# Optimization experiments

Measured on AMD Instinct MI355X. Metric: run time of the kernel, lower is better.

Reference implementation:

```python
import jax, jax.numpy as jnp
import numpy as np

BATCH, HIDDEN, DIM_X, N_FORCING, DIM_T, MODES = 16, 128, 128, 4, 64, 96


def setup_inputs() -> dict:
    key = jax.random.key(0)
    k1, k2, k3, k4, k5 = jax.random.split(key, 5)
    scale = 1.0 / HIDDEN ** 2
    return {
        "z0": jax.random.normal(k1, (BATCH, HIDDEN, DIM_X), jnp.float32),
        "xi": jax.random.normal(k2, (BATCH, N_FORCING, DIM_X, DIM_T), jnp.float32),
        "A": scale * jax.random.uniform(k3, (2, MODES, HIDDEN, HIDDEN), jnp.float32),
        "W_F": jax.random.normal(k4, (HIDDEN, HIDDEN), jnp.float32) / np.sqrt(HIDDEN).astype(np.float32),
        "W_G": jax.random.normal(k5, (HIDDEN, N_FORCING, HIDDEN), jnp.float32) / np.sqrt(HIDDEN).astype(np.float32),
    }


def _spde_func(z, W_F, W_G):
    # z: (b, h, x) -> F_z: (b, h, x), G_z: (b, h, n, x)
    F_z = jnp.tanh(jnp.einsum('oh,bhx->box', W_F, z))
    G_z = jnp.tanh(jnp.einsum('onh,bhx->bonx', W_G, z))
    return F_z, G_z


def _compl_mat_vec_mul_1d(A, z):
    # A: (2, modes, h, h); z: (batch, 2, modes, h) -- (real, imag) stacked on dim 1
    op = lambda M, u: jnp.einsum('xij,bxj->bxi', M, u)
    re = op(A[0], z[:, 0]) - op(A[1], z[:, 1])
    im = op(A[1], z[:, 0]) - op(A[0], z[:, 1])  # faithful to original (minus sign)
    return jnp.stack([re, im], axis=1)


def _prod(v, xi_t, A, W_F, W_G, a, b):
    # v: (batch, 2, dim_x, hidden); xi_t: (batch, dim_x, n_forcing) = dX/dt at step i
    Av = jnp.zeros_like(v).at[:, :, a:b].set(_compl_mat_vec_mul_1d(A, v[:, :, a:b]))
    vc = v[:, 0] + 1j * v[:, 1]                      # (b, x, h) complex
    z = jnp.fft.ifft(jnp.fft.ifftshift(vc, axes=1), axis=1).real  # (b, x, h)
    z = jnp.transpose(z, (0, 2, 1))                  # (b, h, x)
    F_z, G_z = _spde_func(z, W_F, W_G)
    G_z_xi = jnp.einsum('bhnx,bxn->bhx', G_z, xi_t)
    H = F_z + G_z_xi                                 # (b, h, x)
    hf = jnp.fft.fftshift(jnp.fft.fft(H, axis=2), axes=2)
    hf = jnp.stack([hf.real, hf.imag], axis=1)       # (b, 2, h, x)
    hf = jnp.transpose(hf, (0, 1, 3, 2))             # (b, 2, x, h)
    out_ft = jnp.zeros_like(v).at[:, :, a:b].set(hf[:, :, a:b])
    return Av + out_ft


def reference(z0, xi, A, W_F, W_G):
    batch, hidden, dim_x = z0.shape
    modes = A.shape[1]
    a, b = dim_x // 2 - modes // 2, dim_x // 2 + modes // 2
    # v0: band-limited shifted FFT of z0, layout (b, 2, x, h)
    z0_ft = jnp.fft.fftshift(jnp.fft.fft(z0, axis=2), axes=2)
    z0_ft = jnp.stack([z0_ft.real, z0_ft.imag], axis=1)            # (b, 2, h, x)
    v0 = jnp.zeros_like(z0_ft).at[:, :, :, a:b].set(z0_ft[:, :, :, a:b])
    v0 = jnp.transpose(v0, (0, 1, 3, 2))                           # (b, 2, x, h)
    # control increments: linear interp slope on uniform grid t=arange(T), dt=1
    xi_path = jnp.transpose(xi, (0, 2, 3, 1))                      # (b, x, t, n)
    dxi = xi_path[:, :, 1:, :] - xi_path[:, :, :-1, :]             # (b, x, t-1, n)
    dxi = jnp.moveaxis(dxi, 2, 0)                                  # (t-1, b, x, n)

    def step(v, d):
        v_new = v + _prod(v, d, A, W_F, W_G, a, b)  # Euler, dt = 1
        return v_new, v_new

    _, traj = jax.lax.scan(step, v0, dxi)                          # (t-1, b, 2, x, h)
    traj = jnp.concatenate([v0[None], traj], axis=0)               # (t, b, 2, x, h)
    vc = traj[:, :, 0] + 1j * traj[:, :, 1]                        # (t, b, x, h)
    vc = jnp.transpose(vc, (1, 3, 2, 0))                           # (b, h, x, t)
    z = jnp.fft.ifft(jnp.fft.ifftshift(vc, axes=2), axis=2).real   # (b, h, x, t)
    return z
```

## Files before the change

### kernel.cpp

```cpp
#include <hip/hip_runtime.h>
#include <math.h>

#define BATCH 16
#define HID   128
#define NX    128
#define NF    4
#define NT    64
#define MODES 96
#define NWG   256
#define TPB   1024
#define GSZ   16
#define ZSZ   ((size_t)BATCH * NX * HID)

__global__ void k_tables(float* __restrict__ C, float* __restrict__ S,
                         float2* __restrict__ T2m) {
    int m = blockIdx.x, x = threadIdx.x;
    if (x < NX) {
        int k = (80 + m) % NX;
        float ang = (float)((k * x) & (NX - 1)) * (2.0f * (float)M_PI / (float)NX);
        float c = cosf(ang), s = sinf(ang);
        C[m * NX + x] = c;
        S[m * NX + x] = s;
        T2m[m * NX + x] = make_float2(c, s);
    }
}

__global__ void k_dxi(const float* __restrict__ xi, float* __restrict__ dxi) {
    int idx = blockIdx.x * blockDim.x + threadIdx.x;
    const int total = (NT - 1) * BATCH * NX * NF;
    if (idx < total) {
        int n = idx & (NF - 1);
        int x = (idx >> 2) & (NX - 1);
        int b = (idx >> 9) & (BATCH - 1);
        int t = idx >> 13;
        const float* base = xi + (((size_t)b * NF + n) * NX + x) * NT;
        dxi[idx] = base[t + 1] - base[t];
    }
}

__global__ void k_wt4(const float* __restrict__ WF, const float* __restrict__ WGm,
                      float4* __restrict__ Wt4, float* __restrict__ Wt1) {
    int idx = blockIdx.x * 256 + threadIdx.x;
    if (idx < 16 * HID * 8) {
        int ol = idx & 7, h = (idx >> 3) & 127, j = idx >> 10;
        int o = j * 8 + ol;
        Wt4[idx] = make_float4(WF[(size_t)o * HID + h],
                               WGm[((size_t)o * NF + 0) * HID + h],
                               WGm[((size_t)o * NF + 1) * HID + h],
                               WGm[((size_t)o * NF + 2) * HID + h]);
        Wt1[idx] = WGm[((size_t)o * NF + 3) * HID + h];
    }
}

__global__ void k_at2(const float* __restrict__ A, float2* __restrict__ At2) {
    __shared__ float t0[32][33], t1[32][33];
    int m = blockIdx.z;
    int h0 = blockIdx.x * 32, o0 = blockIdx.y * 32;
    int tx = threadIdx.x, ty = threadIdx.y;
    const float* A0 = A + (size_t)m * HID * HID;
    const float* A1 = A0 + (size_t)MODES * HID * HID;
    #pragma unroll
    for (int j = 0; j < 32; j += 8) {
        t0[ty + j][tx] = A0[(size_t)(o0 + ty + j) * HID + h0 + tx];
        t1[ty + j][tx] = A1[(size_t)(o0 + ty + j) * HID + h0 + tx];
    }
    __syncthreads();
    #pragma unroll
    for (int j = 0; j < 32; j += 8)
        At2[((size_t)m * HID + h0 + ty + j) * HID + o0 + tx] =
            make_float2(t0[tx][ty + j], t1[tx][ty + j]);
}

__global__ __launch_bounds__(TPB, 1) void k_solve(
    const float* __restrict__ z0, const float* __restrict__ Ct,
    const float* __restrict__ St, const float2* __restrict__ T2m,
    const float4* __restrict__ Wt4g, const float* __restrict__ Wt1g,
    const float2* __restrict__ At2, const float* __restrict__ dxi,
    float2* __restrict__ va, float2* __restrict__ vb,
    float* __restrict__ zbuf, float* __restrict__ Hc,
    float* __restrict__ out, int* __restrict__ barc)
{
    __shared__ float2 CS[MODES][8];
    __shared__ float  zsl[NX][132];
    __shared__ float4 Wsl4[HID][8];
    __shared__ float  Wsl1[HID][9];
    __shared__ float  dxs[NX][5];
    __shared__ float2 vsl[6][HID];

    const int w = blockIdx.x;
    const int t = threadIdx.x;
    const int b = w >> 4;
    const int j = w & 15;
    const int xg0 = j * 8;
    const int o0 = j * 8;
    const int m0 = j * 6;

    int nbar = 0;
    int* ctr = barc + b * 64;
    auto gbar = [&]() {
        ++nbar;
        __syncthreads();
        if (t == 0) {
            __hip_atomic_fetch_add(ctr, 1, __ATOMIC_RELEASE,
                                   __HIP_MEMORY_SCOPE_AGENT);
            while (__hip_atomic_load(ctr, __ATOMIC_RELAXED,
                                     __HIP_MEMORY_SCOPE_AGENT) < GSZ * nbar)
                __builtin_amdgcn_s_sleep(2);
            (void)__hip_atomic_load(ctr, __ATOMIC_ACQUIRE,
                                    __HIP_MEMORY_SCOPE_AGENT);
        }
        __syncthreads();
    };

    if (t < MODES * 8) {
        int m = t >> 3, xp = t & 7;
        CS[m][xp] = T2m[m * NX + xg0 + xp];
    }
    {
        int h = t >> 3, ol = t & 7;
        Wsl4[h][ol] = Wt4g[((size_t)j * HID + h) * 8 + ol];
        Wsl1[h][ol] = Wt1g[((size_t)j * HID + h) * 8 + ol];
    }

    {
        int h = t & 127, q = t >> 7;
        int c = q & 1, mq = q >> 1;
        const float* zr = z0 + ((size_t)b * HID + h) * NX;
        float* fva = (float*)va;
        #pragma unroll
        for (int jj = 0; jj < 2; ++jj) {
            int mm = mq + 4 * jj;
            if (mm < 6) {
                int m = m0 + mm;
                const float* Trow = (c ? St : Ct) + m * NX;
                float acc = 0.f;
                #pragma unroll 4
                for (int x = 0; x < NX; ++x) acc += zr[x] * Trow[x];
                if (c) acc = -acc;
                fva[(((size_t)b * MODES + m) * HID + h) * 2 + c] = acc;
            }
        }
    }
    gbar();

    float2* vcur = va;
    float2* vnxt = vb;

    for (int step = 0; step < NT; ++step) {
        if (step > 0 && (step & 15) == 0) {
            int t0 = step - 16;
            int xl = t >> 7, h = t & 127;
            int x = xg0 + xl;
            float vals[16];
            #pragma unroll
            for (int tt = 0; tt < 16; ++tt)
                vals[tt] = zbuf[(size_t)tt * ZSZ + ((size_t)b * NX + x) * HID + h];
            float* dst = out + (((size_t)b * HID + h) * NX + x) * NT + t0;
            #pragma unroll
            for (int q = 0; q < 4; ++q)
                ((float4*)dst)[q] = make_float4(vals[q*4], vals[q*4+1],
                                                vals[q*4+2], vals[q*4+3]);
        }

        {
            int h = t & 127, xp = t >> 7;
            const float2* vr = vcur + (size_t)b * MODES * HID + h;
            float acc = 0.f;
            #pragma unroll 4
            for (int m = 0; m < MODES; ++m) {
                float2 vv = vr[(size_t)m * HID];
                float2 cs = CS[m][xp];
                acc += vv.x * cs.x - vv.y * cs.y;
            }
            acc *= 0.0078125f;
            zbuf[(size_t)(step & 15) * ZSZ + ((size_t)b * NX + xg0 + xp) * HID + h] = acc;
        }
        if (step == NT - 1) break;
        gbar();

        {
            const float4* z4 = (const float4*)(zbuf + (size_t)(step & 15) * ZSZ
                                               + (size_t)b * NX * HID);
            #pragma unroll
            for (int k = 0; k < 4; ++k) {
                int idx = t + k * 1024;
                int x = idx >> 5, h4 = (idx & 31) * 4;
                *(float4*)&zsl[x][h4] = z4[idx];
            }
            if (t < 512)
                dxs[t >> 2][t & 3] =
                    dxi[((size_t)step * BATCH + b) * NX * NF + t];
            __syncthreads();

            int ol = t & 7, x = t >> 3;
            float a0 = 0.f, a1 = 0.f, a2 = 0.f, a3 = 0.f, a4 = 0.f;
            #pragma unroll 4
            for (int h = 0; h < HID; ++h) {
                float zv = zsl[x][h];
                float4 w4 = Wsl4[h][ol];
                float w1 = Wsl1[h][ol];
                a0 += w4.x * zv; a1 += w4.y * zv;
                a2 += w4.z * zv; a3 += w4.w * zv;
                a4 += w1 * zv;
            }
            float hv = tanhf(a0)
                     + tanhf(a1) * dxs[x][0]
                     + tanhf(a2) * dxs[x][1]
                     + tanhf(a3) * dxs[x][2]
                     + tanhf(a4) * dxs[x][3];
            Hc[((size_t)b * NX + x) * HID + o0 + ol] = hv;
            __syncthreads();
        }
        gbar();

        {
            if (t < 6 * HID) {
                int ml = t >> 7, h = t & 127;
                vsl[ml][h] = vcur[((size_t)b * MODES + m0 + ml) * HID + h];
            }
            __syncthreads();
            if (t < 768) {
                int o = t & 127, ml = t >> 7;
                int m = m0 + ml;
                const float* hp = Hc + (size_t)b * NX * HID + o;
                const float2* trow = T2m + (size_t)m * NX;
                float fre = 0.f, fim = 0.f;
                #pragma unroll 4
                for (int x = 0; x < NX; ++x) {
                    float hv = hp[(size_t)x * HID];
                    float2 cs = trow[x];
                    fre += hv * cs.x;
                    fim -= hv * cs.y;
                }
                const float2* a2p = At2 + ((size_t)m * HID) * HID + o;
                float are = 0.f, aim = 0.f;
                #pragma unroll 4
                for (int h = 0; h < HID; ++h) {
                    float2 a = a2p[(size_t)h * HID];
                    float2 vv = vsl[ml][h];
                    are += a.x * vv.x - a.y * vv.y;
                    aim += a.y * vv.x - a.x * vv.y;
                }
                float2 vo = vsl[ml][o];
                vnxt[((size_t)b * MODES + m) * HID + o] =
                    make_float2(vo.x + are + fre, vo.y + aim + fim);
            }
            __syncthreads();
        }
        gbar();

        float2* tmp = vcur; vcur = vnxt; vnxt = tmp;
    }

    {
        int xl = t >> 7, h = t & 127;
        int x = xg0 + xl;
        float vals[16];
        #pragma unroll
        for (int tt = 0; tt < 16; ++tt)
            vals[tt] = zbuf[(size_t)tt * ZSZ + ((size_t)b * NX + x) * HID + h];
        float* dst = out + (((size_t)b * HID + h) * NX + x) * NT + 48;
        #pragma unroll
        for (int q = 0; q < 4; ++q)
            ((float4*)dst)[q] = make_float4(vals[q*4], vals[q*4+1],
                                            vals[q*4+2], vals[q*4+3]);
    }
}

extern "C" void kernel_launch(void* const* d_in, const int* in_sizes, int n_in,
                              void* d_out, int out_size, void* d_ws, size_t ws_size,
                              hipStream_t stream) {
    const float* z0 = (const float*)d_in[0];
    const float* xi = (const float*)d_in[1];
    const float* A  = (const float*)d_in[2];
    const float* WF = (const float*)d_in[3];
    const float* WG = (const float*)d_in[4];
    float* out = (float*)d_out;

    float* ws = (float*)d_ws;
    size_t off = 0;
    auto alloc = [&](size_t n) { float* p = ws + off; off += n; return p; };

    float*  Ct   = alloc((size_t)MODES * NX);
    float*  St   = alloc((size_t)MODES * NX);
    float2* T2m  = (float2*)alloc((size_t)MODES * NX * 2);
    float4* Wt4  = (float4*)alloc((size_t)16 * HID * 8 * 4);
    float*  Wt1  = alloc((size_t)16 * HID * 8);
    float2* At2  = (float2*)alloc((size_t)MODES * HID * HID * 2);
    float2* va   = (float2*)alloc((size_t)BATCH * MODES * HID * 2);
    float2* vb   = (float2*)alloc((size_t)BATCH * MODES * HID * 2);
    float*  Hcb  = alloc((size_t)BATCH * NX * HID);
    float*  dxib = alloc((size_t)(NT - 1) * BATCH * NX * NF);
    float*  zbuf = alloc(16 * ZSZ);
    int*    barc = (int*)alloc(BATCH * 64);

    hipMemsetAsync(barc, 0, BATCH * 64 * sizeof(int), stream);
    k_tables<<<MODES, 128, 0, stream>>>(Ct, St, T2m);
    {
        int total = (NT - 1) * BATCH * NX * NF;
        k_dxi<<<(total + 255) / 256, 256, 0, stream>>>(xi, dxib);
    }
    k_wt4<<<64, 256, 0, stream>>>(WF, WG, Wt4, Wt1);
    k_at2<<<dim3(4, 4, MODES), dim3(32, 8), 0, stream>>>(A, At2);

    k_solve<<<NWG, TPB, 0, stream>>>(z0, Ct, St, T2m, Wt4, Wt1, At2, dxib,
                                     va, vb, zbuf, Hcb, out, barc);
}
```

Before: 3.805 ms.

## Pack A weights as bf16 and pair batches per workgroup to share A loads

Stores the spectral mixing matrix A as packed bf16 real/imag pairs, halving the bytes each A-matvec streams from memory. It also regroups workgroups so each group of 32 handles two batch elements, with every workgroup computing 3 modes for both batches. Each A row load is then reused across two batches, and there are 8 barrier groups instead of 16. The cost is lower precision on A and larger barrier groups, which may raise synchronization latency.

```diff
diff --git a/kernel.cpp b/kernel.cpp
--- a/kernel.cpp
+++ b/kernel.cpp
@@ -1,4 +1,5 @@
 #include <hip/hip_runtime.h>
+#include <hip/hip_bf16.h>
 #include <math.h>
 
 #define BATCH 16
@@ -9,7 +10,8 @@
 #define MODES 96
 #define NWG   256
 #define TPB   1024
-#define GSZ   16
+#define NGRP  8
+#define GSZ   32
 #define ZSZ   ((size_t)BATCH * NX * HID)
 
 __global__ void k_tables(float* __restrict__ C, float* __restrict__ S,
@@ -52,7 +54,7 @@
     }
 }
 
-__global__ void k_at2(const float* __restrict__ A, float2* __restrict__ At2) {
+__global__ void k_at2(const float* __restrict__ A, unsigned int* __restrict__ At2b) {
     __shared__ float t0[32][33], t1[32][33];
     int m = blockIdx.z;
     int h0 = blockIdx.x * 32, o0 = blockIdx.y * 32;
@@ -66,16 +68,20 @@
     }
     __syncthreads();
     #pragma unroll
-    for (int j = 0; j < 32; j += 8)
-        At2[((size_t)m * HID + h0 + ty + j) * HID + o0 + tx] =
-            make_float2(t0[tx][ty + j], t1[tx][ty + j]);
+    for (int j = 0; j < 32; j += 8) {
+        __hip_bfloat16 b0 = __float2bfloat16(t0[tx][ty + j]);
+        __hip_bfloat16 b1 = __float2bfloat16(t1[tx][ty + j]);
+        unsigned int u = (unsigned int)(*(unsigned short*)&b0)
+                       | ((unsigned int)(*(unsigned short*)&b1) << 16);
+        At2b[((size_t)m * HID + h0 + ty + j) * HID + o0 + tx] = u;
+    }
 }
 
 __global__ __launch_bounds__(TPB, 1) void k_solve(
     const float* __restrict__ z0, const float* __restrict__ Ct,
     const float* __restrict__ St, const float2* __restrict__ T2m,
     const float4* __restrict__ Wt4g, const float* __restrict__ Wt1g,
-    const float2* __restrict__ At2, const float* __restrict__ dxi,
+    const unsigned int* __restrict__ At2b, const float* __restrict__ dxi,
     float2* __restrict__ va, float2* __restrict__ vb,
     float* __restrict__ zbuf, float* __restrict__ Hc,
     float* __restrict__ out, int* __restrict__ barc)
@@ -85,18 +91,22 @@
     __shared__ float4 Wsl4[HID][8];
     __shared__ float  Wsl1[HID][9];
     __shared__ float  dxs[NX][5];
-    __shared__ float2 vsl[6][HID];
+    __shared__ float2 vsl[2][3][HID];
 
     const int w = blockIdx.x;
     const int t = threadIdx.x;
-    const int b = w >> 4;
-    const int j = w & 15;
-    const int xg0 = j * 8;
-    const int o0 = j * 8;
-    const int m0 = j * 6;
+    const int g = w & 7;
+    const int j = w >> 3;
+    const int jb = j & 1;
+    const int j2 = j >> 1;
+    const int bP = g * 2 + jb;
+    const int xg0 = j2 * 8;
+    const int o0 = j2 * 8;
+    const int m0v = j2 * 6;
+    const int m0 = j * 3;
 
     int nbar = 0;
-    int* ctr = barc + b * 64;
+    int* ctr = barc + g * 64;
     auto gbar = [&]() {
         ++nbar;
         __syncthreads();
@@ -118,26 +128,26 @@
     }
     {
         int h = t >> 3, ol = t & 7;
-        Wsl4[h][ol] = Wt4g[((size_t)j * HID + h) * 8 + ol];
-        Wsl1[h][ol] = Wt1g[((size_t)j * HID + h) * 8 + ol];
+        Wsl4[h][ol] = Wt4g[((size_t)j2 * HID + h) * 8 + ol];
+        Wsl1[h][ol] = Wt1g[((size_t)j2 * HID + h) * 8 + ol];
     }
 
     {
         int h = t & 127, q = t >> 7;
         int c = q & 1, mq = q >> 1;
-        const float* zr = z0 + ((size_t)b * HID + h) * NX;
+        const float* zr = z0 + ((size_t)bP * HID + h) * NX;
         float* fva = (float*)va;
         #pragma unroll
         for (int jj = 0; jj < 2; ++jj) {
             int mm = mq + 4 * jj;
             if (mm < 6) {
-                int m = m0 + mm;
+                int m = m0v + mm;
                 const float* Trow = (c ? St : Ct) + m * NX;
                 float acc = 0.f;
                 #pragma unroll 4
                 for (int x = 0; x < NX; ++x) acc += zr[x] * Trow[x];
                 if (c) acc = -acc;
-                fva[(((size_t)b * MODES + m) * HID + h) * 2 + c] = acc;
+                fva[(((size_t)bP * MODES + m) * HID + h) * 2 + c] = acc;
             }
         }
     }
@@ -154,8 +164,8 @@
             float vals[16];
             #pragma unroll
             for (int tt = 0; tt < 16; ++tt)
-                vals[tt] = zbuf[(size_t)tt * ZSZ + ((size_t)b * NX + x) * HID + h];
-            float* dst = out + (((size_t)b * HID + h) * NX + x) * NT + t0;
+                vals[tt] = zbuf[(size_t)tt * ZSZ + ((size_t)bP * NX + x) * HID + h];
+            float* dst = out + (((size_t)bP * HID + h) * NX + x) * NT + t0;
             #pragma unroll
             for (int q = 0; q < 4; ++q)
                 ((float4*)dst)[q] = make_float4(vals[q*4], vals[q*4+1],
@@ -164,7 +174,7 @@
 
         {
             int h = t & 127, xp = t >> 7;
-            const float2* vr = vcur + (size_t)b * MODES * HID + h;
+            const float2* vr = vcur + (size_t)bP * MODES * HID + h;
             float acc = 0.f;
             #pragma unroll 4
             for (int m = 0; m < MODES; ++m) {
@@ -173,14 +183,14 @@
                 acc += vv.x * cs.x - vv.y * cs.y;
             }
             acc *= 0.0078125f;
-            zbuf[(size_t)(step & 15) * ZSZ + ((size_t)b * NX + xg0 + xp) * HID + h] = acc;
+            zbuf[(size_t)(step & 15) * ZSZ + ((size_t)bP * NX + xg0 + xp) * HID + h] = acc;
         }
         if (step == NT - 1) break;
         gbar();
 
         {
             const float4* z4 = (const float4*)(zbuf + (size_t)(step & 15) * ZSZ
-                                               + (size_t)b * NX * HID);
+                                               + (size_t)bP * NX * HID);
             #pragma unroll
             for (int k = 0; k < 4; ++k) {
                 int idx = t + k * 1024;
@@ -189,7 +199,7 @@
             }
             if (t < 512)
                 dxs[t >> 2][t & 3] =
-                    dxi[((size_t)step * BATCH + b) * NX * NF + t];
+                    dxi[((size_t)step * BATCH + bP) * NX * NF + t];
             __syncthreads();
 
             int ol = t & 7, x = t >> 3;
@@ -208,20 +218,25 @@
                      + tanhf(a2) * dxs[x][1]
                      + tanhf(a3) * dxs[x][2]
                      + tanhf(a4) * dxs[x][3];
-            Hc[((size_t)b * NX + x) * HID + o0 + ol] = hv;
+            Hc[((size_t)bP * NX + x) * HID + o0 + ol] = hv;
             __syncthreads();
         }
         gbar();
 
         {
-            if (t < 6 * HID) {
-                int ml = t >> 7, h = t & 127;
-                vsl[ml][h] = vcur[((size_t)b * MODES + m0 + ml) * HID + h];
+            if (t < 768) {
+                int h = t & 127, r2 = t >> 7;
+                int bl = r2 & 1, ml = r2 >> 1;
+                vsl[bl][ml][h] =
+                    vcur[((size_t)(g * 2 + bl) * MODES + m0 + ml) * HID + h];
             }
             __syncthreads();
-            if (t < 768) {
-                int o = t & 127, ml = t >> 7;
+            int r = t >> 7;
+            if (r < 6) {
+                int o = t & 127;
+                int ml = r >> 1, bl = r & 1;
                 int m = m0 + ml;
+                int b = g * 2 + bl;
                 const float* hp = Hc + (size_t)b * NX * HID + o;
                 const float2* trow = T2m + (size_t)m * NX;
                 float fre = 0.f, fim = 0.f;
@@ -232,16 +247,18 @@
                     fre += hv * cs.x;
                     fim -= hv * cs.y;
                 }
-                const float2* a2p = At2 + ((size_t)m * HID) * HID + o;
+                const unsigned int* a2p = At2b + ((size_t)m * HID) * HID + o;
                 float are = 0.f, aim = 0.f;
                 #pragma unroll 4
                 for (int h = 0; h < HID; ++h) {
-                    float2 a = a2p[(size_t)h * HID];
-                    float2 vv = vsl[ml][h];
-                    are += a.x * vv.x - a.y * vv.y;
-                    aim += a.y * vv.x - a.x * vv.y;
+                    unsigned int u = a2p[(size_t)h * HID];
+                    float ax = __uint_as_float((u & 0xffffu) << 16);
+                    float ay = __uint_as_float(u & 0xffff0000u);
+                    float2 vv = vsl[bl][ml][h];
+                    are += ax * vv.x - ay * vv.y;
+                    aim += ay * vv.x - ax * vv.y;
                 }
-                float2 vo = vsl[ml][o];
+                float2 vo = vsl[bl][ml][o];
                 vnxt[((size_t)b * MODES + m) * HID + o] =
                     make_float2(vo.x + are + fre, vo.y + aim + fim);
             }
@@ -258,8 +275,8 @@
         float vals[16];
         #pragma unroll
         for (int tt = 0; tt < 16; ++tt)
-            vals[tt] = zbuf[(size_t)tt * ZSZ + ((size_t)b * NX + x) * HID + h];
-        float* dst = out + (((size_t)b * HID + h) * NX + x) * NT + 48;
+            vals[tt] = zbuf[(size_t)tt * ZSZ + ((size_t)bP * NX + x) * HID + h];
+        float* dst = out + (((size_t)bP * HID + h) * NX + x) * NT + 48;
         #pragma unroll
         for (int q = 0; q < 4; ++q)
             ((float4*)dst)[q] = make_float4(vals[q*4], vals[q*4+1],
@@ -286,23 +303,23 @@
     float2* T2m  = (float2*)alloc((size_t)MODES * NX * 2);
     float4* Wt4  = (float4*)alloc((size_t)16 * HID * 8 * 4);
     float*  Wt1  = alloc((size_t)16 * HID * 8);
-    float2* At2  = (float2*)alloc((size_t)MODES * HID * HID * 2);
+    unsigned int* At2b = (unsigned int*)alloc((size_t)MODES * HID * HID);
     float2* va   = (float2*)alloc((size_t)BATCH * MODES * HID * 2);
     float2* vb   = (float2*)alloc((size_t)BATCH * MODES * HID * 2);
     float*  Hcb  = alloc((size_t)BATCH * NX * HID);
     float*  dxib = alloc((size_t)(NT - 1) * BATCH * NX * NF);
     float*  zbuf = alloc(16 * ZSZ);
-    int*    barc = (int*)alloc(BATCH * 64);
-
-    hipMemsetAsync(barc, 0, BATCH * 64 * sizeof(int), stream);
+    int*    barc = (int*)alloc(NGRP * 64);
+
+    hipMemsetAsync(barc, 0, NGRP * 64 * sizeof(int), stream);
     k_tables<<<MODES, 128, 0, stream>>>(Ct, St, T2m);
     {
         int total = (NT - 1) * BATCH * NX * NF;
         k_dxi<<<(total + 255) / 256, 256, 0, stream>>>(xi, dxib);
     }
     k_wt4<<<64, 256, 0, stream>>>(WF, WG, Wt4, Wt1);
-    k_at2<<<dim3(4, 4, MODES), dim3(32, 8), 0, stream>>>(A, At2);
-
-    k_solve<<<NWG, TPB, 0, stream>>>(z0, Ct, St, T2m, Wt4, Wt1, At2, dxib,
+    k_at2<<<dim3(4, 4, MODES), dim3(32, 8), 0, stream>>>(A, At2b);
+
+    k_solve<<<NWG, TPB, 0, stream>>>(z0, Ct, St, T2m, Wt4, Wt1, At2b, dxib,
                                      va, vb, zbuf, Hcb, out, barc);
 }
```

After: 3.958 ms. 4.0% more time.
